# Kernel optimization log

Hardware: AMD Instinct MI355X
Metric: run time of the kernel (lower is better)

Reference implementation:

```python
import jax, jax.numpy as jnp
import numpy as np

B = 4; PER = 32768; N = B * PER
D = 128; G = 128; H = 8; HD = D // H
SPARSE = (32, 360, 360)   # (z, y, x)
WIN = (12, 12, 32)        # (win_x, win_y, win_z) per get_window_coors_shift_v2 unpacking


def setup_inputs() -> dict:
    key = jax.random.key(0)
    ks = jax.random.split(key, 6)
    b = jnp.repeat(jnp.arange(B, dtype=jnp.int32), PER)
    z = jax.random.randint(ks[0], (N,), 0, SPARSE[0], dtype=jnp.int32)
    y = jax.random.randint(ks[1], (N,), 0, SPARSE[1], dtype=jnp.int32)
    x = jax.random.randint(ks[2], (N,), 0, SPARSE[2], dtype=jnp.int32)
    coords = jnp.stack([b, z, y, x], axis=1)  # [N,4]
    feats = jax.random.normal(ks[3], (N, D), dtype=jnp.float32)
    s = 1.0 / np.sqrt(D)
    Wqkv = (jax.random.normal(ks[4], (2, D, 3 * D), dtype=jnp.float32) * s)
    Wo = (jax.random.normal(ks[5], (2, D, D), dtype=jnp.float32) * s)
    ln_g = jnp.ones((2, D), dtype=jnp.float32)
    ln_b = jnp.zeros((2, D), dtype=jnp.float32)
    return dict(coords=coords, feats=feats, Wqkv=Wqkv, Wo=Wo, ln_g=ln_g, ln_b=ln_b)


def _window_keys(coords):
    # Faithful to get_window_coors_shift_v2 (shift=False) + v2 key construction.
    sz, sy, sx = SPARSE
    wx_s, wy_s, wz_s = WIN
    nwx = int(np.ceil(sx / wx_s) + 1)
    nwy = int(np.ceil(sy / wy_s) + 1)
    nwz = int(np.ceil(sz / wz_s) + 1)
    mpw = nwx * nwy * nwz
    vol = wx_s * wy_s * wz_s
    b = coords[:, 0]; z = coords[:, 1]; y = coords[:, 2]; x = coords[:, 3]
    wx = x // wx_s; wy = y // wy_s; wz = z // wz_s
    cx = x % wx_s; cy = y % wy_s; cz = z % wz_s
    bwi_x = b * mpw + wx * (nwy * nwz) + wy * nwz + wz
    bwi_y = b * mpw + wy * (nwx * nwz) + wx * nwz + wz
    vx = bwi_x * vol + cx * (wy_s * wz_s) + cy * wz_s + cz
    vy = bwi_y * vol + cy * (wx_s * wz_s) + cx * wz_s + cz
    return vx, vy


def _layernorm(x, g, b, eps=1e-5):
    mu = jnp.mean(x, axis=-1, keepdims=True)
    var = jnp.var(x, axis=-1, keepdims=True)
    return (x - mu) * jax.lax.rsqrt(var + eps) * g + b


def _group_block(xg, Wqkv, Wo, g, b):
    # xg: [Ng, G, D] grouped window features; pre-LN MHSA with residual.
    Ng = xg.shape[0]
    h = _layernorm(xg, g, b)
    qkv = jnp.einsum('ngd,de->nge', h, Wqkv)             # [Ng,G,3D]
    q, k, v = jnp.split(qkv, 3, axis=-1)
    q = q.reshape(Ng, G, H, HD); k = k.reshape(Ng, G, H, HD); v = v.reshape(Ng, G, H, HD)
    scores = jnp.einsum('nqhd,nkhd->nhqk', q, k) / np.sqrt(HD)
    attn = jax.nn.softmax(scores, axis=-1)
    out = jnp.einsum('nhqk,nkhd->nqhd', attn, v).reshape(Ng, G, D)
    out = jnp.einsum('ngd,de->nge', out, Wo)
    return xg + out


def reference(coords, feats, Wqkv, Wo, ln_g, ln_b):
    vx, vy = _window_keys(coords)
    orders = [jnp.argsort(vx), jnp.argsort(vy)]  # 'x' then 'y' direction
    x = feats
    for i in range(2):
        idx = orders[i]
        xg = x[idx].reshape(-1, G, D)                    # gather + group (flat2win is identity here)
        xg = _group_block(xg, Wqkv[i], Wo[i], ln_g[i], ln_b[i])
        x = x.at[idx].set(xg.reshape(-1, D))             # scatter back (win2flat identity)
    return x
```

## Files before the change

kernel.cpp:

```cpp
#include <hip/hip_runtime.h>
#include <hip/hip_bf16.h>

#define N_TOK 131072
#define NCHUNK 1024
#define NBINS 8192
#define HSTR 8448

typedef __bf16 bf16_t;
typedef bf16_t bf16x4 __attribute__((ext_vector_type(4)));
typedef bf16_t bf16x8 __attribute__((ext_vector_type(8)));
typedef float f32x4 __attribute__((ext_vector_type(4)));
typedef float f32x16 __attribute__((ext_vector_type(16)));

__device__ __forceinline__ unsigned pkbf(float a, float b) {
  unsigned r;
  asm("v_cvt_pk_bf16_f32 %0, %1, %2" : "=v"(r) : "v"(a), "v"(b));
  return r;
}
__device__ __forceinline__ void pl32swap(unsigned& x, unsigned& y) {
  asm("v_permlane32_swap_b32 %0, %1" : "+v"(x), "+v"(y));
}
__device__ __forceinline__ int fra(int frow, int colb) {
  return (frow >> 3) * 272 + (frow & 7) * 32 + colb;
}

__device__ __forceinline__ void win_keys(int b, int z, int y, int x, int r,
                                         int& bwi, int& cell) {
  int wx = x / 12, wy = y / 12, wz = z >> 5;
  int cx = x % 12, cy = y % 12, cz = z & 31;
  if (r == 0) { bwi = b * 1922 + wx * 62 + wy * 2 + wz; cell = cx * 384 + cy * 32 + cz; }
  else        { bwi = b * 1922 + wy * 62 + wx * 2 + wz; cell = cy * 384 + cx * 32 + cz; }
}

__global__ void k_prep(const float* __restrict__ Wqkv, const float* __restrict__ Wo,
                       bf16_t* __restrict__ Wt, bf16_t* __restrict__ Wot) {
  int t = blockIdx.x * 256 + threadIdx.x;
  if (t < 98304) {
    int i = t / 49152, rem = t % 49152, n = rem / 128, k = rem % 128;
    float v = Wqkv[(i * 128 + k) * 384 + n];
    if (n < 128) v *= 0.36067376022224085f;
    Wt[t] = (bf16_t)v;
  } else {
    int u = t - 98304;
    int i = u / 16384, rem = u % 16384, e = rem / 128, d = rem % 128;
    Wot[u] = (bf16_t)Wo[(i * 128 + d) * 128 + e];
  }
}

__global__ void k_hist(const int* __restrict__ coords, int* __restrict__ hist) {
  int t = blockIdx.x * 256 + threadIdx.x;
  int4 c = ((const int4*)coords)[t];
  int bwi, cell;
  win_keys(c.x, c.y, c.z, c.w, 0, bwi, cell);
  atomicAdd(&hist[bwi], 1);
  win_keys(c.x, c.y, c.z, c.w, 1, bwi, cell);
  atomicAdd(&hist[HSTR + bwi], 1);
}

__global__ void k_scan(const int* __restrict__ histb, int* __restrict__ startsb,
                       int* __restrict__ curb) {
  int r = blockIdx.x;
  const int* hist = histb + r * HSTR;
  int* starts = startsb + r * HSTR;
  int* cur = curb + r * HSTR;
  __shared__ int ssum[256];
  int tid = threadIdx.x;
  int base = tid * 32;
  int s = 0;
  for (int j = 0; j < 32; j++) s += hist[base + j];
  ssum[tid] = s;
  __syncthreads();
  if (tid == 0) {
    int acc = 0;
    for (int i = 0; i < 256; i++) { int v = ssum[i]; ssum[i] = acc; acc += v; }
  }
  __syncthreads();
  int run = ssum[tid];
  for (int j = 0; j < 32; j++) {
    starts[base + j] = run; cur[base + j] = run; run += hist[base + j];
  }
  if (tid == 255) starts[NBINS] = run;
}

__global__ void k_scatter(const int* __restrict__ coords, int* __restrict__ cur,
                          int* __restrict__ seg) {
  int t = blockIdx.x * 256 + threadIdx.x;
  int4 c = ((const int4*)coords)[t];
  int bwi, cell;
  win_keys(c.x, c.y, c.z, c.w, 0, bwi, cell);
  seg[atomicAdd(&cur[bwi], 1)] = (cell << 17) | t;
  win_keys(c.x, c.y, c.z, c.w, 1, bwi, cell);
  seg[N_TOK + atomicAdd(&cur[HSTR + bwi], 1)] = (cell << 17) | t;
}

__global__ void k_winsort(const int* __restrict__ startsb, const int* __restrict__ segb,
                          int* __restrict__ orderb) {
  int r = blockIdx.y;
  const int* starts = startsb + r * HSTR;
  const int* seg = segb + r * N_TOK;
  int* order = orderb + r * N_TOK;
  int w = blockIdx.x;
  int s = starts[w], m = starts[w + 1] - s;
  for (int i = threadIdx.x; i < m; i += 256) {
    int v = seg[s + i], rk = 0;
    for (int j = 0; j < m; j++) rk += (seg[s + j] < v);
    order[s + rk] = v & 0x1FFFF;
  }
}

#define VSW(d) ((((d) >> 3) & 7) << 4)
__global__ __launch_bounds__(512, 4) void k_fused(
    const bf16_t* __restrict__ Wt, const bf16_t* __restrict__ Wot,
    const int* __restrict__ order, const float* __restrict__ ln_g,
    const float* __restrict__ ln_b, const float* __restrict__ xin,
    float* __restrict__ xout) {
  int chunk = blockIdx.x;
  __shared__ bf16_t hL[128 * 136];
  __shared__ bf16_t vT[128 * 136];
  char* hLb = (char*)hL;
  int tid = threadIdx.x, wv = tid >> 6, lane = tid & 63;
  int l16 = lane & 15, gk = 8 * (lane >> 4), r4 = (lane >> 4) * 4;
  int l31 = lane & 31, hi = lane >> 5;

  {
    int row = tid >> 2, g = tid & 3;
    int tok = order[chunk * 128 + row];
    const float4* src = (const float4*)(xin + (size_t)tok * 128) + g * 8;
    float4 v[8];
    #pragma unroll
    for (int j = 0; j < 8; j++) v[j] = src[j];
    float s = 0.f, sq = 0.f;
    #pragma unroll
    for (int j = 0; j < 8; j++) {
      s += v[j].x + v[j].y + v[j].z + v[j].w;
      sq += v[j].x * v[j].x + v[j].y * v[j].y + v[j].z * v[j].z + v[j].w * v[j].w;
    }
    s += __shfl_xor(s, 1); sq += __shfl_xor(sq, 1);
    s += __shfl_xor(s, 2); sq += __shfl_xor(sq, 2);
    float mean = s * 0.0078125f;
    float var = sq * 0.0078125f - mean * mean;
    float rstd = rsqrtf(var + 1e-5f);
    #pragma unroll
    for (int j = 0; j < 8; j++) {
      float4 gv = ((const float4*)ln_g)[g * 8 + j];
      float4 bv = ((const float4*)ln_b)[g * 8 + j];
      bf16x4 o;
      o[0] = (bf16_t)((v[j].x - mean) * rstd * gv.x + bv.x);
      o[1] = (bf16_t)((v[j].y - mean) * rstd * gv.y + bv.y);
      o[2] = (bf16_t)((v[j].z - mean) * rstd * gv.z + bv.z);
      o[3] = (bf16_t)((v[j].w - mean) * rstd * gv.w + bv.w);
      *(bf16x4*)(&hL[row * 136 + g * 32 + j * 4]) = o;
    }
  }
  __syncthreads();

  {
    int wr = wv >> 2, wc = wv & 3;
    f32x4 acc[4][2] = {};
    #pragma unroll
    for (int ks = 0; ks < 4; ks++) {
      int k0 = ks * 32 + gk;
      bf16x8 a[4], b[2];
      #pragma unroll
      for (int mi = 0; mi < 4; mi++)
        a[mi] = *(const bf16x8*)(&hL[(wr * 64 + mi * 16 + l16) * 136 + k0]);
      #pragma unroll
      for (int ni = 0; ni < 2; ni++)
        b[ni] = *(const bf16x8*)(Wt + (size_t)(256 + wc * 32 + ni * 16 + l16) * 128 + k0);
      #pragma unroll
      for (int mi = 0; mi < 4; mi++)
        #pragma unroll
        for (int ni = 0; ni < 2; ni++)
          acc[mi][ni] = __builtin_amdgcn_mfma_f32_16x16x32_bf16(a[mi], b[ni], acc[mi][ni], 0, 0, 0);
    }
    #pragma unroll
    for (int mi = 0; mi < 4; mi++)
      #pragma unroll
      for (int ni = 0; ni < 2; ni++) {
        int d = wc * 32 + ni * 16 + l16;
        int tok0 = wr * 64 + mi * 16 + r4;
        bf16x4 o;
        #pragma unroll
        for (int e = 0; e < 4; e++) o[e] = (bf16_t)acc[mi][ni][e];
        *(bf16x4*)((char*)vT + ((d * 272 + tok0 * 2) ^ VSW(d))) = o;
      }
  }

  uint2 px[4][4];
  int wrA = wv >> 1, wcA = wv & 1;
  {
    f32x4 acc[4][4] = {};
    #pragma unroll
    for (int ks = 0; ks < 4; ks++) {
      int k0 = ks * 32 + gk;
      bf16x8 a[4], b[4];
      #pragma unroll
      for (int mi = 0; mi < 4; mi++)
        a[mi] = *(const bf16x8*)(Wt + (size_t)(wrA * 64 + mi * 16 + l16) * 128 + k0);
      #pragma unroll
      for (int ni = 0; ni < 4; ni++)
        b[ni] = *(const bf16x8*)(&hL[(wcA * 64 + ni * 16 + l16) * 136 + k0]);
      #pragma unroll
      for (int mi = 0; mi < 4; mi++)
        #pragma unroll
        for (int ni = 0; ni < 4; ni++)
          acc[mi][ni] = __builtin_amdgcn_mfma_f32_16x16x32_bf16(a[mi], b[ni], acc[mi][ni], 0, 0, 0);
    }
    #pragma unroll
    for (int mi = 0; mi < 4; mi++)
      #pragma unroll
      for (int ni = 0; ni < 4; ni++) {
        bf16x4 o;
        #pragma unroll
        for (int e = 0; e < 4; e++) o[e] = (bf16_t)acc[mi][ni][e];
        px[mi][ni] = __builtin_bit_cast(uint2, o);
      }
  }
  __syncthreads();

  bool isK = (wv >= 4);
  if (isK) {
    #pragma unroll
    for (int mi = 0; mi < 4; mi++)
      #pragma unroll
      for (int ni = 0; ni < 4; ni++) {
        int n = wrA * 64 + mi * 16 + r4;
        int tok = wcA * 64 + ni * 16 + l16;
        int head = (n >> 4) & 7;
        *(uint2*)(hLb + fra(head * 128 + tok, (n & 15) * 2)) = px[mi][ni];
      }
  }
  __syncthreads();
  bf16x8 kf[4];
  #pragma unroll
  for (int kt = 0; kt < 4; kt++)
    kf[kt] = *(const bf16x8*)(hLb + fra(wv * 128 + 32 * kt + l31, hi * 16));
  __syncthreads();
  if (!isK) {
    #pragma unroll
    for (int mi = 0; mi < 4; mi++)
      #pragma unroll
      for (int ni = 0; ni < 4; ni++) {
        int n = wrA * 64 + mi * 16 + r4;
        int tok = wcA * 64 + ni * 16 + l16;
        int head = (n >> 4) & 7;
        *(uint2*)(hLb + fra(head * 128 + tok, (n & 15) * 2)) = px[mi][ni];
      }
  }
  __syncthreads();

  {
    int dvt = wv * 16 + (l31 & 15);
    #pragma unroll 1
    for (int qt = 0; qt < 4; qt++) {
      bf16x8 qf = *(const bf16x8*)(hLb + fra(wv * 128 + 32 * qt + l31, hi * 16));
      f32x16 sc[4];
      __builtin_amdgcn_s_setprio(1);
      #pragma unroll
      for (int kt = 0; kt < 4; kt++) {
        f32x16 z = {};
        sc[kt] = __builtin_amdgcn_mfma_f32_32x32x16_bf16(kf[kt], qf, z, 0, 0, 0);
      }
      __builtin_amdgcn_s_setprio(0);
      float sum = 0.f;
      uint4 pfw[8];
      #pragma unroll
      for (int s = 0; s < 8; s++) {
        int t = s >> 1, sl = (s & 1) * 8;
        float p0 = __builtin_amdgcn_exp2f(sc[t][sl + 0]);
        float p1 = __builtin_amdgcn_exp2f(sc[t][sl + 1]);
        float p2 = __builtin_amdgcn_exp2f(sc[t][sl + 2]);
        float p3 = __builtin_amdgcn_exp2f(sc[t][sl + 3]);
        float p4 = __builtin_amdgcn_exp2f(sc[t][sl + 4]);
        float p5 = __builtin_amdgcn_exp2f(sc[t][sl + 5]);
        float p6 = __builtin_amdgcn_exp2f(sc[t][sl + 6]);
        float p7 = __builtin_amdgcn_exp2f(sc[t][sl + 7]);
        sum += ((p0 + p1) + (p2 + p3)) + ((p4 + p5) + (p6 + p7));
        unsigned X0 = pkbf(p0, p1), X1 = pkbf(p2, p3);
        unsigned Y0 = pkbf(p4, p5), Y1 = pkbf(p6, p7);
        pl32swap(X0, Y0);
        pl32swap(X1, Y1);
        pfw[s] = (uint4){X0, X1, Y0, Y1};
      }
      sum += __shfl_xor(sum, 32);
      float inv = 1.0f / sum;
      f32x16 C = {};
      __builtin_amdgcn_s_setprio(1);
      #pragma unroll
      for (int s = 0; s < 8; s++) {
        bf16x8 pf = __builtin_bit_cast(bf16x8, pfw[s]);
        bf16x8 vf = *(const bf16x8*)((const char*)vT +
                     ((dvt * 272 + (16 * s + 8 * hi) * 2) ^ VSW(dvt)));
        C = __builtin_amdgcn_mfma_f32_32x32x16_bf16(pf, vf, C, 0, 0, 0);
      }
      __builtin_amdgcn_s_setprio(0);
      #pragma unroll
      for (int e = 0; e < 16; e++) {
        int row = (e & 3) + 8 * (e >> 2) + 4 * hi;
        float rsv = __shfl(inv, row, 32);
        if (l31 < 16)
          *(bf16_t*)(hLb + fra(wv * 128 + 32 * qt + row, l31 * 2)) =
              (bf16_t)(C[e] * rsv);
      }
    }
  }
  __syncthreads();

  {
    int wr = wv >> 2, wc = wv & 3;
    int qr = wr * 64, qc = wc * 32;
    f32x4 acc[4][2] = {};
    #pragma unroll
    for (int ks = 0; ks < 4; ks++) {
      int k0 = ks * 32 + gk;
      bf16x8 a[4], b[2];
      #pragma unroll
      for (int mi = 0; mi < 4; mi++)
        a[mi] = *(const bf16x8*)(hLb +
                 fra((k0 >> 4) * 128 + (qr + mi * 16 + l16), (k0 & 8) * 2));
      #pragma unroll
      for (int ni = 0; ni < 2; ni++)
        b[ni] = *(const bf16x8*)(Wot + (qc + ni * 16 + l16) * 128 + k0);
      #pragma unroll
      for (int mi = 0; mi < 4; mi++)
        #pragma unroll
        for (int ni = 0; ni < 2; ni++)
          acc[mi][ni] = __builtin_amdgcn_mfma_f32_16x16x32_bf16(a[mi], b[ni], acc[mi][ni], 0, 0, 0);
    }
    #pragma unroll
    for (int mi = 0; mi < 4; mi++) {
      #pragma unroll
      for (int e = 0; e < 4; e++) {
        int row = qr + mi * 16 + r4 + e;
        int tok = order[chunk * 128 + row];
        #pragma unroll
        for (int ni = 0; ni < 2; ni++) {
          int col = qc + ni * 16 + l16;
          xout[(size_t)tok * 128 + col] = xin[(size_t)tok * 128 + col] + acc[mi][ni][e];
        }
      }
    }
  }
}

extern "C" void kernel_launch(void* const* d_in, const int* in_sizes, int n_in,
                              void* d_out, int out_size, void* d_ws, size_t ws_size,
                              hipStream_t stream) {
  const int* coords = (const int*)d_in[0];
  const float* feats = (const float*)d_in[1];
  const float* Wqkv = (const float*)d_in[2];
  const float* Wo = (const float*)d_in[3];
  const float* ln_g = (const float*)d_in[4];
  const float* ln_b = (const float*)d_in[5];
  float* out = (float*)d_out;

  char* w = (char*)d_ws;
  size_t off = 0;
  auto take = [&](size_t b) { char* p = w + off; off += (b + 255) & ~(size_t)255; return p; };
  int* hist   = (int*)take(2 * HSTR * 4);
  int* starts = (int*)take(2 * HSTR * 4);
  int* cur    = (int*)take(2 * HSTR * 4);
  int* seg    = (int*)take(2 * (size_t)N_TOK * 4);
  int* order  = (int*)take(2 * (size_t)N_TOK * 4);
  bf16_t* Wt  = (bf16_t*)take(2 * 384 * 128 * 2);
  bf16_t* Wot = (bf16_t*)take(2 * 128 * 128 * 2);

  k_prep<<<512, 256, 0, stream>>>(Wqkv, Wo, Wt, Wot);
  hipMemsetAsync(hist, 0, 2 * HSTR * 4, stream);
  k_hist<<<512, 256, 0, stream>>>(coords, hist);
  k_scan<<<2, 256, 0, stream>>>(hist, starts, cur);
  k_scatter<<<512, 256, 0, stream>>>(coords, cur, seg);
  k_winsort<<<dim3(NBINS, 2), 256, 0, stream>>>(starts, seg, order);

  for (int r = 0; r < 2; r++) {
    const float* xin = (r == 0) ? feats : out;
    k_fused<<<NCHUNK, 512, 0, stream>>>(Wt + r * 49152, Wot + r * 16384,
                                        order + r * N_TOK, ln_g + r * 128,
                                        ln_b + r * 128, xin, out);
  }
}
```

Baseline: 237.6 us.

## Process two chunks per block with prefetch of next chunk's features

Each fused block now handles two 128-token chunks and loads the second chunk's gathered features into registers during the first chunk's attention, hiding the global gather latency. The weight-prep and histogram kernels are merged into one launch. Barriers are replaced by an lgkmcnt-wait plus raw s_barrier, and the softmax/PV loop is split into two score groups to lower register pressure. The cost is a grid halved to 512 blocks and higher register use from the prefetch buffer, which may reduce occupancy.

```diff
diff --git a/kernel.cpp b/kernel.cpp
--- a/kernel.cpp
+++ b/kernel.cpp
@@ -19,6 +19,11 @@
 }
 __device__ __forceinline__ void pl32swap(unsigned& x, unsigned& y) {
   asm("v_permlane32_swap_b32 %0, %1" : "+v"(x), "+v"(y));
+}
+__device__ __forceinline__ void bar_lgkm() {
+  asm volatile("s_waitcnt lgkmcnt(0)" ::: "memory");
+  __builtin_amdgcn_s_barrier();
+  __builtin_amdgcn_sched_barrier(0);
 }
 __device__ __forceinline__ int fra(int frow, int colb) {
   return (frow >> 3) * 272 + (frow & 7) * 32 + colb;
@@ -32,8 +37,9 @@
   else        { bwi = b * 1922 + wy * 62 + wx * 2 + wz; cell = cy * 384 + cx * 32 + cz; }
 }
 
-__global__ void k_prep(const float* __restrict__ Wqkv, const float* __restrict__ Wo,
-                       bf16_t* __restrict__ Wt, bf16_t* __restrict__ Wot) {
+__global__ void k_pre(const float* __restrict__ Wqkv, const float* __restrict__ Wo,
+                      const int* __restrict__ coords, bf16_t* __restrict__ Wt,
+                      bf16_t* __restrict__ Wot, int* __restrict__ hist) {
   int t = blockIdx.x * 256 + threadIdx.x;
   if (t < 98304) {
     int i = t / 49152, rem = t % 49152, n = rem / 128, k = rem % 128;
@@ -45,10 +51,6 @@
     int i = u / 16384, rem = u % 16384, e = rem / 128, d = rem % 128;
     Wot[u] = (bf16_t)Wo[(i * 128 + d) * 128 + e];
   }
-}
-
-__global__ void k_hist(const int* __restrict__ coords, int* __restrict__ hist) {
-  int t = blockIdx.x * 256 + threadIdx.x;
   int4 c = ((const int4*)coords)[t];
   int bwi, cell;
   win_keys(c.x, c.y, c.z, c.w, 0, bwi, cell);
@@ -114,232 +116,252 @@
     const int* __restrict__ order, const float* __restrict__ ln_g,
     const float* __restrict__ ln_b, const float* __restrict__ xin,
     float* __restrict__ xout) {
-  int chunk = blockIdx.x;
   __shared__ bf16_t hL[128 * 136];
   __shared__ bf16_t vT[128 * 136];
   char* hLb = (char*)hL;
   int tid = threadIdx.x, wv = tid >> 6, lane = tid & 63;
   int l16 = lane & 15, gk = 8 * (lane >> 4), r4 = (lane >> 4) * 4;
   int l31 = lane & 31, hi = lane >> 5;
-
+  int row4 = tid >> 2, g4 = tid & 3;
+
+  float4 pv[8];
+  int tokp = order[blockIdx.x * 128 + row4];
   {
-    int row = tid >> 2, g = tid & 3;
-    int tok = order[chunk * 128 + row];
-    const float4* src = (const float4*)(xin + (size_t)tok * 128) + g * 8;
-    float4 v[8];
+    const float4* src = (const float4*)(xin + (size_t)tokp * 128) + g4 * 8;
     #pragma unroll
-    for (int j = 0; j < 8; j++) v[j] = src[j];
-    float s = 0.f, sq = 0.f;
+    for (int j = 0; j < 8; j++) pv[j] = src[j];
+  }
+
+  #pragma unroll
+  for (int half = 0; half < 2; half++) {
+    int chunk = blockIdx.x + half * 512;
+
+    {
+      float s = 0.f, sq = 0.f;
+      #pragma unroll
+      for (int j = 0; j < 8; j++) {
+        s += pv[j].x + pv[j].y + pv[j].z + pv[j].w;
+        sq += pv[j].x * pv[j].x + pv[j].y * pv[j].y + pv[j].z * pv[j].z + pv[j].w * pv[j].w;
+      }
+      s += __shfl_xor(s, 1); sq += __shfl_xor(sq, 1);
+      s += __shfl_xor(s, 2); sq += __shfl_xor(sq, 2);
+      float mean = s * 0.0078125f;
+      float var = sq * 0.0078125f - mean * mean;
+      float rstd = rsqrtf(var + 1e-5f);
+      #pragma unroll
+      for (int j = 0; j < 8; j++) {
+        float4 gv = ((const float4*)ln_g)[g4 * 8 + j];
+        float4 bv = ((const float4*)ln_b)[g4 * 8 + j];
+        bf16x4 o;
+        o[0] = (bf16_t)((pv[j].x - mean) * rstd * gv.x + bv.x);
+        o[1] = (bf16_t)((pv[j].y - mean) * rstd * gv.y + bv.y);
+        o[2] = (bf16_t)((pv[j].z - mean) * rstd * gv.z + bv.z);
+        o[3] = (bf16_t)((pv[j].w - mean) * rstd * gv.w + bv.w);
+        *(bf16x4*)(&hL[row4 * 136 + g4 * 32 + j * 4]) = o;
+      }
+    }
+    bar_lgkm();
+
+    {
+      int wr = wv >> 2, wc = wv & 3;
+      f32x4 acc[4][2] = {};
+      #pragma unroll
+      for (int ks = 0; ks < 4; ks++) {
+        int k0 = ks * 32 + gk;
+        bf16x8 a[4], b[2];
+        #pragma unroll
+        for (int mi = 0; mi < 4; mi++)
+          a[mi] = *(const bf16x8*)(&hL[(wr * 64 + mi * 16 + l16) * 136 + k0]);
+        #pragma unroll
+        for (int ni = 0; ni < 2; ni++)
+          b[ni] = *(const bf16x8*)(Wt + (size_t)(256 + wc * 32 + ni * 16 + l16) * 128 + k0);
+        #pragma unroll
+        for (int mi = 0; mi < 4; mi++)
+          #pragma unroll
+          for (int ni = 0; ni < 2; ni++)
+            acc[mi][ni] = __builtin_amdgcn_mfma_f32_16x16x32_bf16(a[mi], b[ni], acc[mi][ni], 0, 0, 0);
+      }
+      #pragma unroll
+      for (int mi = 0; mi < 4; mi++)
+        #pragma unroll
+        for (int ni = 0; ni < 2; ni++) {
+          int d = wc * 32 + ni * 16 + l16;
+          int tok0 = wr * 64 + mi * 16 + r4;
+          bf16x4 o;
+          #pragma unroll
+          for (int e = 0; e < 4; e++) o[e] = (bf16_t)acc[mi][ni][e];
+          *(bf16x4*)((char*)vT + ((d * 272 + tok0 * 2) ^ VSW(d))) = o;
+        }
+    }
+
+    uint2 px[4][4];
+    int wrA = wv >> 1, wcA = wv & 1;
+    {
+      f32x4 acc[4][4] = {};
+      #pragma unroll
+      for (int ks = 0; ks < 4; ks++) {
+        int k0 = ks * 32 + gk;
+        bf16x8 a[4], b[4];
+        #pragma unroll
+        for (int mi = 0; mi < 4; mi++)
+          a[mi] = *(const bf16x8*)(Wt + (size_t)(wrA * 64 + mi * 16 + l16) * 128 + k0);
+        #pragma unroll
+        for (int ni = 0; ni < 4; ni++)
+          b[ni] = *(const bf16x8*)(&hL[(wcA * 64 + ni * 16 + l16) * 136 + k0]);
+        #pragma unroll
+        for (int mi = 0; mi < 4; mi++)
+          #pragma unroll
+          for (int ni = 0; ni < 4; ni++)
+            acc[mi][ni] = __builtin_amdgcn_mfma_f32_16x16x32_bf16(a[mi], b[ni], acc[mi][ni], 0, 0, 0);
+      }
+      #pragma unroll
+      for (int mi = 0; mi < 4; mi++)
+        #pragma unroll
+        for (int ni = 0; ni < 4; ni++) {
+          bf16x4 o;
+          #pragma unroll
+          for (int e = 0; e < 4; e++) o[e] = (bf16_t)acc[mi][ni][e];
+          px[mi][ni] = __builtin_bit_cast(uint2, o);
+        }
+    }
+    bar_lgkm();
+
+    bool isK = (wv >= 4);
+    if (isK) {
+      #pragma unroll
+      for (int mi = 0; mi < 4; mi++)
+        #pragma unroll
+        for (int ni = 0; ni < 4; ni++) {
+          int n = wrA * 64 + mi * 16 + r4;
+          int tok = wcA * 64 + ni * 16 + l16;
+          int head = (n >> 4) & 7;
+          *(uint2*)(hLb + fra(head * 128 + tok, (n & 15) * 2)) = px[mi][ni];
+        }
+    }
+    bar_lgkm();
+    bf16x8 kf[4];
     #pragma unroll
-    for (int j = 0; j < 8; j++) {
-      s += v[j].x + v[j].y + v[j].z + v[j].w;
-      sq += v[j].x * v[j].x + v[j].y * v[j].y + v[j].z * v[j].z + v[j].w * v[j].w;
-    }
-    s += __shfl_xor(s, 1); sq += __shfl_xor(sq, 1);
-    s += __shfl_xor(s, 2); sq += __shfl_xor(sq, 2);
-    float mean = s * 0.0078125f;
-    float var = sq * 0.0078125f - mean * mean;
-    float rstd = rsqrtf(var + 1e-5f);
-    #pragma unroll
-    for (int j = 0; j < 8; j++) {
-      float4 gv = ((const float4*)ln_g)[g * 8 + j];
-      float4 bv = ((const float4*)ln_b)[g * 8 + j];
-      bf16x4 o;
-      o[0] = (bf16_t)((v[j].x - mean) * rstd * gv.x + bv.x);
-      o[1] = (bf16_t)((v[j].y - mean) * rstd * gv.y + bv.y);
-      o[2] = (bf16_t)((v[j].z - mean) * rstd * gv.z + bv.z);
-      o[3] = (bf16_t)((v[j].w - mean) * rstd * gv.w + bv.w);
-      *(bf16x4*)(&hL[row * 136 + g * 32 + j * 4]) = o;
-    }
-  }
-  __syncthreads();
-
-  {
-    int wr = wv >> 2, wc = wv & 3;
-    f32x4 acc[4][2] = {};
-    #pragma unroll
-    for (int ks = 0; ks < 4; ks++) {
-      int k0 = ks * 32 + gk;
-      bf16x8 a[4], b[2];
+    for (int kt = 0; kt < 4; kt++)
+      kf[kt] = *(const bf16x8*)(hLb + fra(wv * 128 + 32 * kt + l31, hi * 16));
+    bar_lgkm();
+    if (!isK) {
       #pragma unroll
       for (int mi = 0; mi < 4; mi++)
-        a[mi] = *(const bf16x8*)(&hL[(wr * 64 + mi * 16 + l16) * 136 + k0]);
-      #pragma unroll
-      for (int ni = 0; ni < 2; ni++)
-        b[ni] = *(const bf16x8*)(Wt + (size_t)(256 + wc * 32 + ni * 16 + l16) * 128 + k0);
-      #pragma unroll
-      for (int mi = 0; mi < 4; mi++)
+        #pragma unroll
+        for (int ni = 0; ni < 4; ni++) {
+          int n = wrA * 64 + mi * 16 + r4;
+          int tok = wcA * 64 + ni * 16 + l16;
+          int head = (n >> 4) & 7;
+          *(uint2*)(hLb + fra(head * 128 + tok, (n & 15) * 2)) = px[mi][ni];
+        }
+    }
+    bar_lgkm();
+
+    if (half == 0) {
+      tokp = order[(blockIdx.x + 512) * 128 + row4];
+      const float4* src = (const float4*)(xin + (size_t)tokp * 128) + g4 * 8;
+      #pragma unroll
+      for (int j = 0; j < 8; j++) pv[j] = src[j];
+    }
+
+    {
+      int dvt = wv * 16 + (l31 & 15);
+      #pragma unroll 1
+      for (int qt = 0; qt < 4; qt++) {
+        bf16x8 qf = *(const bf16x8*)(hLb + fra(wv * 128 + 32 * qt + l31, hi * 16));
+        float sum = 0.f;
+        f32x16 C = {};
+        #pragma unroll
+        for (int g = 0; g < 2; g++) {
+          f32x16 sc0, sc1;
+          __builtin_amdgcn_s_setprio(1);
+          {
+            f32x16 z0 = {}, z1 = {};
+            sc0 = __builtin_amdgcn_mfma_f32_32x32x16_bf16(kf[2 * g], qf, z0, 0, 0, 0);
+            sc1 = __builtin_amdgcn_mfma_f32_32x32x16_bf16(kf[2 * g + 1], qf, z1, 0, 0, 0);
+          }
+          __builtin_amdgcn_s_setprio(0);
+          uint4 pfw[4];
+          #pragma unroll
+          for (int j = 0; j < 4; j++) {
+            const f32x16& sct = (j < 2) ? sc0 : sc1;
+            int sl = (j & 1) * 8;
+            float p0 = __builtin_amdgcn_exp2f(sct[sl + 0]);
+            float p1 = __builtin_amdgcn_exp2f(sct[sl + 1]);
+            float p2 = __builtin_amdgcn_exp2f(sct[sl + 2]);
+            float p3 = __builtin_amdgcn_exp2f(sct[sl + 3]);
+            float p4 = __builtin_amdgcn_exp2f(sct[sl + 4]);
+            float p5 = __builtin_amdgcn_exp2f(sct[sl + 5]);
+            float p6 = __builtin_amdgcn_exp2f(sct[sl + 6]);
+            float p7 = __builtin_amdgcn_exp2f(sct[sl + 7]);
+            sum += ((p0 + p1) + (p2 + p3)) + ((p4 + p5) + (p6 + p7));
+            unsigned X0 = pkbf(p0, p1), X1 = pkbf(p2, p3);
+            unsigned Y0 = pkbf(p4, p5), Y1 = pkbf(p6, p7);
+            pl32swap(X0, Y0);
+            pl32swap(X1, Y1);
+            pfw[j] = (uint4){X0, X1, Y0, Y1};
+          }
+          __builtin_amdgcn_s_setprio(1);
+          #pragma unroll
+          for (int j = 0; j < 4; j++) {
+            int s = 4 * g + j;
+            bf16x8 pf = __builtin_bit_cast(bf16x8, pfw[j]);
+            bf16x8 vf = *(const bf16x8*)((const char*)vT +
+                         ((dvt * 272 + (16 * s + 8 * hi) * 2) ^ VSW(dvt)));
+            C = __builtin_amdgcn_mfma_f32_32x32x16_bf16(pf, vf, C, 0, 0, 0);
+          }
+          __builtin_amdgcn_s_setprio(0);
+        }
+        sum += __shfl_xor(sum, 32);
+        float inv = 1.0f / sum;
+        #pragma unroll
+        for (int e = 0; e < 16; e++) {
+          int row = (e & 3) + 8 * (e >> 2) + 4 * hi;
+          float rsv = __shfl(inv, row, 32);
+          if (l31 < 16)
+            *(bf16_t*)(hLb + fra(wv * 128 + 32 * qt + row, l31 * 2)) =
+                (bf16_t)(C[e] * rsv);
+        }
+      }
+    }
+    bar_lgkm();
+
+    {
+      int wr = wv >> 2, wc = wv & 3;
+      int qr = wr * 64, qc = wc * 32;
+      f32x4 acc[4][2] = {};
+      #pragma unroll
+      for (int ks = 0; ks < 4; ks++) {
+        int k0 = ks * 32 + gk;
+        bf16x8 a[4], b[2];
+        #pragma unroll
+        for (int mi = 0; mi < 4; mi++)
+          a[mi] = *(const bf16x8*)(hLb +
+                   fra((k0 >> 4) * 128 + (qr + mi * 16 + l16), (k0 & 8) * 2));
         #pragma unroll
         for (int ni = 0; ni < 2; ni++)
-          acc[mi][ni] = __builtin_amdgcn_mfma_f32_16x16x32_bf16(a[mi], b[ni], acc[mi][ni], 0, 0, 0);
-    }
-    #pragma unroll
-    for (int mi = 0; mi < 4; mi++)
-      #pragma unroll
-      for (int ni = 0; ni < 2; ni++) {
-        int d = wc * 32 + ni * 16 + l16;
-        int tok0 = wr * 64 + mi * 16 + r4;
-        bf16x4 o;
-        #pragma unroll
-        for (int e = 0; e < 4; e++) o[e] = (bf16_t)acc[mi][ni][e];
-        *(bf16x4*)((char*)vT + ((d * 272 + tok0 * 2) ^ VSW(d))) = o;
-      }
-  }
-
-  uint2 px[4][4];
-  int wrA = wv >> 1, wcA = wv & 1;
-  {
-    f32x4 acc[4][4] = {};
-    #pragma unroll
-    for (int ks = 0; ks < 4; ks++) {
-      int k0 = ks * 32 + gk;
-      bf16x8 a[4], b[4];
-      #pragma unroll
-      for (int mi = 0; mi < 4; mi++)
-        a[mi] = *(const bf16x8*)(Wt + (size_t)(wrA * 64 + mi * 16 + l16) * 128 + k0);
-      #pragma unroll
-      for (int ni = 0; ni < 4; ni++)
-        b[ni] = *(const bf16x8*)(&hL[(wcA * 64 + ni * 16 + l16) * 136 + k0]);
-      #pragma unroll
-      for (int mi = 0; mi < 4; mi++)
-        #pragma unroll
-        for (int ni = 0; ni < 4; ni++)
-          acc[mi][ni] = __builtin_amdgcn_mfma_f32_16x16x32_bf16(a[mi], b[ni], acc[mi][ni], 0, 0, 0);
-    }
-    #pragma unroll
-    for (int mi = 0; mi < 4; mi++)
-      #pragma unroll
-      for (int ni = 0; ni < 4; ni++) {
-        bf16x4 o;
-        #pragma unroll
-        for (int e = 0; e < 4; e++) o[e] = (bf16_t)acc[mi][ni][e];
-        px[mi][ni] = __builtin_bit_cast(uint2, o);
-      }
-  }
-  __syncthreads();
-
-  bool isK = (wv >= 4);
-  if (isK) {
-    #pragma unroll
-    for (int mi = 0; mi < 4; mi++)
-      #pragma unroll
-      for (int ni = 0; ni < 4; ni++) {
-        int n = wrA * 64 + mi * 16 + r4;
-        int tok = wcA * 64 + ni * 16 + l16;
-        int head = (n >> 4) & 7;
-        *(uint2*)(hLb + fra(head * 128 + tok, (n & 15) * 2)) = px[mi][ni];
-      }
-  }
-  __syncthreads();
-  bf16x8 kf[4];
-  #pragma unroll
-  for (int kt = 0; kt < 4; kt++)
-    kf[kt] = *(const bf16x8*)(hLb + fra(wv * 128 + 32 * kt + l31, hi * 16));
-  __syncthreads();
-  if (!isK) {
-    #pragma unroll
-    for (int mi = 0; mi < 4; mi++)
-      #pragma unroll
-      for (int ni = 0; ni < 4; ni++) {
-        int n = wrA * 64 + mi * 16 + r4;
-        int tok = wcA * 64 + ni * 16 + l16;
-        int head = (n >> 4) & 7;
-        *(uint2*)(hLb + fra(head * 128 + tok, (n & 15) * 2)) = px[mi][ni];
-      }
-  }
-  __syncthreads();
-
-  {
-    int dvt = wv * 16 + (l31 & 15);
-    #pragma unroll 1
-    for (int qt = 0; qt < 4; qt++) {
-      bf16x8 qf = *(const bf16x8*)(hLb + fra(wv * 128 + 32 * qt + l31, hi * 16));
-      f32x16 sc[4];
-      __builtin_amdgcn_s_setprio(1);
-      #pragma unroll
-      for (int kt = 0; kt < 4; kt++) {
-        f32x16 z = {};
-        sc[kt] = __builtin_amdgcn_mfma_f32_32x32x16_bf16(kf[kt], qf, z, 0, 0, 0);
-      }
-      __builtin_amdgcn_s_setprio(0);
-      float sum = 0.f;
-      uint4 pfw[8];
-      #pragma unroll
-      for (int s = 0; s < 8; s++) {
-        int t = s >> 1, sl = (s & 1) * 8;
-        float p0 = __builtin_amdgcn_exp2f(sc[t][sl + 0]);
-        float p1 = __builtin_amdgcn_exp2f(sc[t][sl + 1]);
-        float p2 = __builtin_amdgcn_exp2f(sc[t][sl + 2]);
-        float p3 = __builtin_amdgcn_exp2f(sc[t][sl + 3]);
-        float p4 = __builtin_amdgcn_exp2f(sc[t][sl + 4]);
-        float p5 = __builtin_amdgcn_exp2f(sc[t][sl + 5]);
-        float p6 = __builtin_amdgcn_exp2f(sc[t][sl + 6]);
-        float p7 = __builtin_amdgcn_exp2f(sc[t][sl + 7]);
-        sum += ((p0 + p1) + (p2 + p3)) + ((p4 + p5) + (p6 + p7));
-        unsigned X0 = pkbf(p0, p1), X1 = pkbf(p2, p3);
-        unsigned Y0 = pkbf(p4, p5), Y1 = pkbf(p6, p7);
-        pl32swap(X0, Y0);
-        pl32swap(X1, Y1);
-        pfw[s] = (uint4){X0, X1, Y0, Y1};
-      }
-      sum += __shfl_xor(sum, 32);
-      float inv = 1.0f / sum;
-      f32x16 C = {};
-      __builtin_amdgcn_s_setprio(1);
-      #pragma unroll
-      for (int s = 0; s < 8; s++) {
-        bf16x8 pf = __builtin_bit_cast(bf16x8, pfw[s]);
-        bf16x8 vf = *(const bf16x8*)((const char*)vT +
-                     ((dvt * 272 + (16 * s + 8 * hi) * 2) ^ VSW(dvt)));
-        C = __builtin_amdgcn_mfma_f32_32x32x16_bf16(pf, vf, C, 0, 0, 0);
-      }
-      __builtin_amdgcn_s_setprio(0);
-      #pragma unroll
-      for (int e = 0; e < 16; e++) {
-        int row = (e & 3) + 8 * (e >> 2) + 4 * hi;
-        float rsv = __shfl(inv, row, 32);
-        if (l31 < 16)
-          *(bf16_t*)(hLb + fra(wv * 128 + 32 * qt + row, l31 * 2)) =
-              (bf16_t)(C[e] * rsv);
-      }
-    }
-  }
-  __syncthreads();
-
-  {
-    int wr = wv >> 2, wc = wv & 3;
-    int qr = wr * 64, qc = wc * 32;
-    f32x4 acc[4][2] = {};
-    #pragma unroll
-    for (int ks = 0; ks < 4; ks++) {
-      int k0 = ks * 32 + gk;
-      bf16x8 a[4], b[2];
-      #pragma unroll
-      for (int mi = 0; mi < 4; mi++)
-        a[mi] = *(const bf16x8*)(hLb +
-                 fra((k0 >> 4) * 128 + (qr + mi * 16 + l16), (k0 & 8) * 2));
-      #pragma unroll
-      for (int ni = 0; ni < 2; ni++)
-        b[ni] = *(const bf16x8*)(Wot + (qc + ni * 16 + l16) * 128 + k0);
-      #pragma unroll
-      for (int mi = 0; mi < 4; mi++)
-        #pragma unroll
-        for (int ni = 0; ni < 2; ni++)
-          acc[mi][ni] = __builtin_amdgcn_mfma_f32_16x16x32_bf16(a[mi], b[ni], acc[mi][ni], 0, 0, 0);
-    }
-    #pragma unroll
-    for (int mi = 0; mi < 4; mi++) {
-      #pragma unroll
-      for (int e = 0; e < 4; e++) {
-        int row = qr + mi * 16 + r4 + e;
-        int tok = order[chunk * 128 + row];
-        #pragma unroll
-        for (int ni = 0; ni < 2; ni++) {
-          int col = qc + ni * 16 + l16;
-          xout[(size_t)tok * 128 + col] = xin[(size_t)tok * 128 + col] + acc[mi][ni][e];
-        }
-      }
-    }
+          b[ni] = *(const bf16x8*)(Wot + (qc + ni * 16 + l16) * 128 + k0);
+        #pragma unroll
+        for (int mi = 0; mi < 4; mi++)
+          #pragma unroll
+          for (int ni = 0; ni < 2; ni++)
+            acc[mi][ni] = __builtin_amdgcn_mfma_f32_16x16x32_bf16(a[mi], b[ni], acc[mi][ni], 0, 0, 0);
+      }
+      #pragma unroll
+      for (int mi = 0; mi < 4; mi++) {
+        #pragma unroll
+        for (int e = 0; e < 4; e++) {
+          int row = qr + mi * 16 + r4 + e;
+          int tok = order[chunk * 128 + row];
+          #pragma unroll
+          for (int ni = 0; ni < 2; ni++) {
+            int col = qc + ni * 16 + l16;
+            xout[(size_t)tok * 128 + col] = xin[(size_t)tok * 128 + col] + acc[mi][ni][e];
+          }
+        }
+      }
+    }
+    if (half == 0) bar_lgkm();
   }
 }
 
@@ -365,17 +387,16 @@
   bf16_t* Wt  = (bf16_t*)take(2 * 384 * 128 * 2);
   bf16_t* Wot = (bf16_t*)take(2 * 128 * 128 * 2);
 
-  k_prep<<<512, 256, 0, stream>>>(Wqkv, Wo, Wt, Wot);
   hipMemsetAsync(hist, 0, 2 * HSTR * 4, stream);
-  k_hist<<<512, 256, 0, stream>>>(coords, hist);
+  k_pre<<<512, 256, 0, stream>>>(Wqkv, Wo, coords, Wt, Wot, hist);
   k_scan<<<2, 256, 0, stream>>>(hist, starts, cur);
   k_scatter<<<512, 256, 0, stream>>>(coords, cur, seg);
   k_winsort<<<dim3(NBINS, 2), 256, 0, stream>>>(starts, seg, order);
 
   for (int r = 0; r < 2; r++) {
     const float* xin = (r == 0) ? feats : out;
-    k_fused<<<NCHUNK, 512, 0, stream>>>(Wt + r * 49152, Wot + r * 16384,
-                                        order + r * N_TOK, ln_g + r * 128,
-                                        ln_b + r * 128, xin, out);
-  }
-}
+    k_fused<<<512, 512, 0, stream>>>(Wt + r * 49152, Wot + r * 16384,
+                                     order + r * N_TOK, ln_g + r * 128,
+                                     ln_b + r * 128, xin, out);
+  }
+}
```

Result: slower. 305.4 us (+28.5%).
